# Kernel tuning notes

Hardware: AMD Instinct MI355X
Metric: run time of the kernel (lower is better)

Reference implementation:

```python
import jax, jax.numpy as jnp
import numpy as np

B, S, D, H = 2, 2048, 1024, 16
HD = D // H          # 64
ROT = HD // 2        # 32

def _rope(x, cos, sin):
    # x: [B,S,H,HD] -> pairs [B,S,H,ROT,2]; cos/sin: [S,ROT] -> [1,S,1,ROT]
    x2 = x.reshape(x.shape[:3] + (ROT, 2))
    x0, x1 = x2[..., 0], x2[..., 1]
    c = cos[None, :, None, :]
    s = sin[None, :, None, :]
    out = jnp.stack([x0 * c - x1 * s, x1 * c + x0 * s], axis=-1)
    return out.reshape(x.shape)

def setup_inputs() -> dict:
    key = jax.random.key(0)
    ks = jax.random.split(key, 5)
    hidden_states = jax.random.normal(ks[0], (B, S, D), dtype=jnp.float32)
    # proper rotary cos/sin table: [S, ROT, 2]
    inv_freq = 1.0 / (10000.0 ** (np.arange(0, ROT, dtype=np.float32) / ROT))
    t = np.arange(S, dtype=np.float32)
    ang = np.outer(t, inv_freq)  # [S, ROT]
    freqs = jnp.asarray(np.stack([np.cos(ang), np.sin(ang)], axis=-1), dtype=jnp.float32)
    sc = 1.0 / np.sqrt(D)
    wq = jax.random.normal(ks[1], (D, D), dtype=jnp.float32) * sc
    wk = jax.random.normal(ks[2], (D, D), dtype=jnp.float32) * sc
    wv = jax.random.normal(ks[3], (D, D), dtype=jnp.float32) * sc
    wo = jax.random.normal(ks[4], (D, D), dtype=jnp.float32) * sc
    return {"hidden_states": hidden_states, "freqs": freqs, "wq": wq, "wk": wk, "wv": wv, "wo": wo}

def reference(hidden_states, freqs, wq, wk, wv, wo):
    b, s, _ = hidden_states.shape
    scaling = HD ** -0.5
    q = (hidden_states @ wq.T).reshape(b, s, H, HD)
    k = (hidden_states @ wk.T).reshape(b, s, H, HD)
    v = (hidden_states @ wv.T).reshape(b, s, H, HD)
    cos, sin = freqs[:s, :, 0], freqs[:s, :, 1]
    q = _rope(q, cos, sin)
    k = _rope(k, cos, sin)
    # [B,H,S,S] scores, fp32 softmax
    scores = jnp.einsum('bqhd,bkhd->bhqk', q, k) * scaling
    attn = jax.nn.softmax(scores.astype(jnp.float32), axis=-1).astype(q.dtype)
    out = jnp.einsum('bhqk,bkhd->bqhd', attn, v).reshape(b, s, D)
    return out @ wo.T
```

## Files before the change

kernel.cpp:

```cpp
#include <hip/hip_runtime.h>
#include <hip/hip_bf16.h>

typedef __attribute__((ext_vector_type(8))) short bf16x8;
typedef __attribute__((ext_vector_type(4))) float f32x4;
typedef __attribute__((ext_vector_type(16))) float f32x16;
typedef __attribute__((ext_vector_type(2))) float f32x2;
typedef unsigned short u16;

#define Bc   2
#define Sc   2048
#define Dc   1024
#define Hc   16
#define HDc  64
#define ROTc 32
#define Mrows 4096

__device__ __forceinline__ u16 f2bf(float x) {
  union { float f; unsigned u; } v{x};
  unsigned r = v.u + 0x7fffu + ((v.u >> 16) & 1u);
  return (u16)(r >> 16);
}
__device__ __forceinline__ float bf2f(u16 x) {
  union { unsigned u; float f; } v{(unsigned)x << 16};
  return v.f;
}
__device__ __forceinline__ unsigned cvtpk(float a, float b) {
  unsigned r;
  asm("v_cvt_pk_bf16_f32 %0, %1, %2" : "=v"(r) : "v"(a), "v"(b));
  return r;
}
__device__ __forceinline__ f32x2 pmax2(f32x2 a, f32x2 b) {
  f32x2 r;
  r.x = fmaxf(a.x, b.x);
  r.y = fmaxf(a.y, b.y);
  return r;
}

__device__ __forceinline__ void gload_lds16(const void* g, void* l) {
  __builtin_amdgcn_global_load_lds(
      (const __attribute__((address_space(1))) void*)g,
      (__attribute__((address_space(3))) void*)l, 16, 0, 0);
}

__global__ void cvt_all(const float* __restrict__ h, const float* __restrict__ q,
                        const float* __restrict__ k, const float* __restrict__ v,
                        const float* __restrict__ o,
                        u16* __restrict__ hb, u16* __restrict__ qb, u16* __restrict__ kb,
                        u16* __restrict__ vb, u16* __restrict__ ob) {
  size_t i = ((size_t)blockIdx.x * 256 + threadIdx.x) * 4;
  const float* s;
  u16* d;
  size_t off;
  if (i < (size_t)Mrows * Dc) {
    s = h; d = hb; off = i;
  } else {
    size_t j = i - (size_t)Mrows * Dc;
    int w = (int)(j >> 20);
    off = j & ((1u << 20) - 1);
    s = (w == 0) ? q : (w == 1) ? k : (w == 2) ? v : o;
    d = (w == 0) ? qb : (w == 1) ? kb : (w == 2) ? vb : ob;
  }
  float4 val = *reinterpret_cast<const float4*>(s + off);
  u16 r0 = f2bf(val.x), r1 = f2bf(val.y), r2 = f2bf(val.z), r3 = f2bf(val.w);
  ushort4 outv = {r0, r1, r2, r3};
  *reinterpret_cast<ushort4*>(d + off) = outv;
}

__global__ void gemm_qkv(const u16* __restrict__ A, const u16* __restrict__ W0,
                         const u16* __restrict__ W1, const u16* __restrict__ W2,
                         const float* __restrict__ freqs,
                         u16* __restrict__ Qo, u16* __restrict__ Ko,
                         u16* __restrict__ Vo) {
  __shared__ u16 As[128 * 32];
  __shared__ u16 Bs[128 * 32];
  const int by = blockIdx.y;
  const int wsel = by >> 3;
  const int n0 = (by & 7) * 128;
  const int m0 = blockIdx.x * 128;
  const u16* Bm = (wsel == 0) ? W0 : (wsel == 1) ? W1 : W2;
  const int t = threadIdx.x;
  const int w = t >> 6;
  const int lane = t & 63;
  const int wm = w >> 1, wn = w & 1;
  const int c = lane & 15, g = lane >> 4;
  const int srow = t >> 2, skoff = (t & 3) * 8;

  f32x4 acc[4][4] = {};

  const u16* ag = A + (size_t)(m0 + srow) * Dc + skoff;
  const u16* bg = Bm + (size_t)(n0 + srow) * Dc + skoff;
  u16* al = &As[(w * 16) * 32];
  u16* bl = &Bs[(w * 16) * 32];

  for (int k0 = 0; k0 < Dc; k0 += 32) {
    gload_lds16(ag + k0, al);
    gload_lds16(ag + k0 + (size_t)64 * Dc, al + 64 * 32);
    gload_lds16(bg + k0, bl);
    gload_lds16(bg + k0 + (size_t)64 * Dc, bl + 64 * 32);
    __syncthreads();
    bf16x8 a[4], b[4];
#pragma unroll
    for (int f = 0; f < 4; ++f) {
      a[f] = *(const bf16x8*)&As[(wm * 64 + f * 16 + c) * 32 + g * 8];
      b[f] = *(const bf16x8*)&Bs[(wn * 64 + f * 16 + c) * 32 + g * 8];
    }
#pragma unroll
    for (int fm = 0; fm < 4; ++fm)
#pragma unroll
      for (int fn = 0; fn < 4; ++fn)
        acc[fm][fn] =
            __builtin_amdgcn_mfma_f32_16x16x32_bf16(a[fm], b[fn], acc[fm][fn], 0, 0, 0);
    __syncthreads();
  }

  u16* dst = (wsel == 0) ? Qo : (wsel == 1) ? Ko : Vo;
  const float qsc = (wsel == 0) ? 0.125f * 1.44269504f : 1.0f;
  const int codd = c & 1;
#pragma unroll
  for (int fm = 0; fm < 4; ++fm)
#pragma unroll
    for (int fn = 0; fn < 4; ++fn)
#pragma unroll
      for (int r = 0; r < 4; ++r) {
        const int m = m0 + wm * 64 + fm * 16 + g * 4 + r;
        const int n = n0 + wn * 64 + fn * 16 + c;
        float v = acc[fm][fn][r];
        const int b = m >> 11, s = m & (Sc - 1);
        const int hh = n >> 6, d = n & 63;
        size_t idx;
        if (wsel < 2) {
          const float other = __shfl_xor(v, 1);
          const float2 f = reinterpret_cast<const float2*>(freqs)[s * ROTc + (d >> 1)];
          v = codd ? (v * f.x + other * f.y) : (v * f.x - other * f.y);
          v *= qsc;
          idx = (((size_t)(b * Hc + hh) * Sc) + s) * HDc + d;
        } else {
          idx = ((size_t)(b * Hc + hh) * HDc + d) * Sc + s;
        }
        dst[idx] = f2bf(v);
      }
}

__global__ void gemm_out(const u16* __restrict__ A, const u16* __restrict__ Bm,
                         float* __restrict__ C) {
  __shared__ u16 As[64 * 32];
  __shared__ u16 Bs[128 * 32];
  const int m0 = blockIdx.x * 64;
  const int n0 = blockIdx.y * 128;
  const int t = threadIdx.x;
  const int w = t >> 6;
  const int lane = t & 63;
  const int wm = w >> 1, wn = w & 1;
  const int c = lane & 15, g = lane >> 4;
  const int srow = t >> 2, skoff = (t & 3) * 8;

  f32x4 acc[2][4] = {};

  const u16* ag = A + (size_t)(m0 + srow) * Dc + skoff;
  const u16* bg = Bm + (size_t)(n0 + srow) * Dc + skoff;
  u16* al = &As[(w * 16) * 32];
  u16* bl = &Bs[(w * 16) * 32];

  for (int k0 = 0; k0 < Dc; k0 += 32) {
    gload_lds16(ag + k0, al);
    gload_lds16(bg + k0, bl);
    gload_lds16(bg + k0 + (size_t)64 * Dc, bl + 64 * 32);
    __syncthreads();
    bf16x8 a[2], b[4];
#pragma unroll
    for (int f = 0; f < 2; ++f)
      a[f] = *(const bf16x8*)&As[(wm * 32 + f * 16 + c) * 32 + g * 8];
#pragma unroll
    for (int f = 0; f < 4; ++f)
      b[f] = *(const bf16x8*)&Bs[(wn * 64 + f * 16 + c) * 32 + g * 8];
#pragma unroll
    for (int fm = 0; fm < 2; ++fm)
#pragma unroll
      for (int fn = 0; fn < 4; ++fn)
        acc[fm][fn] =
            __builtin_amdgcn_mfma_f32_16x16x32_bf16(a[fm], b[fn], acc[fm][fn], 0, 0, 0);
    __syncthreads();
  }

#pragma unroll
  for (int fm = 0; fm < 2; ++fm)
#pragma unroll
    for (int fn = 0; fn < 4; ++fn)
#pragma unroll
      for (int r = 0; r < 4; ++r) {
        const int m = m0 + wm * 32 + fm * 16 + g * 4 + r;
        const int n = n0 + wn * 64 + fn * 16 + c;
        C[(size_t)m * Dc + n] = acc[fm][fn][r];
      }
}

__global__ __launch_bounds__(512, 2) void flash_attn(
    const u16* __restrict__ Q, const u16* __restrict__ Kb,
    const u16* __restrict__ Vt, u16* __restrict__ Ob) {
  __shared__ u16 smem[32768];
  const int orig = blockIdx.x;
  const int wg = (orig & 7) * 64 + (orig >> 3);
  const int bh = wg >> 4;
  const int q0 = (wg & 15) * 128;
  const int t = threadIdx.x, w = t >> 6, lane = t & 63;
  const int grp = w >> 2, wl = w & 3;
  const int ts = t & 255;
  const int l31 = lane & 31, hi = lane >> 5;
  const int sr = ts >> 4;
  const int su = (ts & 15) ^ (sr & 15);
  const int skv = sr + ((su >> 3) << 5);
  const int sd8 = (su & 7) * 8;
  const int rsw = (l31 & 15);

  const u16* Qp = Q + (size_t)bh * Sc * HDc;
  const u16* Kp = Kb + (size_t)bh * Sc * HDc;
  const u16* Vp = Vt + (size_t)bh * HDc * Sc;
  u16* const Kg = smem + grp * 8192;
  u16* const Vg = smem + 16384 + grp * 8192;

  const int q = q0 + wl * 32 + l31;
  bf16x8 aq[4];
#pragma unroll
  for (int kd = 0; kd < 4; ++kd)
    aq[kd] = *(const bf16x8*)(Qp + (size_t)q * HDc + kd * 16 + hi * 8);

  float m_run = -1e30f, l_run = 0.f;
  f32x16 o0 = {}, o1 = {};

  auto STAGE = [&](int tile, int bb) {
    const int base = grp * 1024 + tile * 64;
    gload_lds16(Kp + (size_t)(base + skv) * HDc + sd8, Kg + bb * 4096 + wl * 512);
    gload_lds16(Kp + (size_t)(base + skv + 16) * HDc + sd8,
                Kg + bb * 4096 + 2048 + wl * 512);
    gload_lds16(Vp + (size_t)skv * Sc + base + sd8, Vg + bb * 4096 + wl * 512);
    gload_lds16(Vp + (size_t)(skv + 16) * Sc + base + sd8,
                Vg + bb * 4096 + 2048 + wl * 512);
  };

  STAGE(0, 0);
  __syncthreads();

  int buf = 0;
  for (int tt = 0; tt < 16; ++tt) {
    if (tt + 1 < 16) STAGE(tt + 1, buf ^ 1);
    const u16* kb2 = Kg + buf * 4096;
    const u16* vb2 = Vg + buf * 4096;
    f32x16 s0 = {}, s1 = {};
    __builtin_amdgcn_s_setprio(1);
#pragma unroll
    for (int kd = 0; kd < 4; ++kd) {
      const int u0 = kd * 2 + hi;
      bf16x8 a0 = *(const bf16x8*)&kb2[l31 * 128 + (u0 ^ rsw) * 8];
      bf16x8 a1 = *(const bf16x8*)&kb2[l31 * 128 + ((u0 + 8) ^ rsw) * 8];
      s0 = __builtin_amdgcn_mfma_f32_32x32x16_bf16(a0, aq[kd], s0, 0, 0, 0);
      s1 = __builtin_amdgcn_mfma_f32_32x32x16_bf16(a1, aq[kd], s1, 0, 0, 0);
    }
    __builtin_amdgcn_s_setprio(0);
    f32x2 t4[4];
#pragma unroll
    for (int i = 0; i < 4; ++i) {
      f32x2 e0; e0.x = s0[2 * i]; e0.y = s0[2 * i + 1];
      f32x2 e1; e1.x = s0[2 * i + 8]; e1.y = s0[2 * i + 9];
      f32x2 e2; e2.x = s1[2 * i]; e2.y = s1[2 * i + 1];
      f32x2 e3; e3.x = s1[2 * i + 8]; e3.y = s1[2 * i + 9];
      t4[i] = pmax2(pmax2(e0, e1), pmax2(e2, e3));
    }
    f32x2 tp = pmax2(pmax2(t4[0], t4[1]), pmax2(t4[2], t4[3]));
    float mt = fmaxf(tp.x, tp.y);
    mt = fmaxf(mt, __shfl_xor(mt, 32));
    const bool skip = __all(mt <= m_run + 8.0f);
    if (!skip) {
      const float mn2 = fmaxf(m_run, mt);
      const float scl = __builtin_amdgcn_exp2f(m_run - mn2);
      m_run = mn2;
      l_run *= scl;
      o0 *= scl;
      o1 *= scl;
    }
    const float mn = m_run;
#pragma unroll
    for (int r = 0; r < 16; ++r) {
      s0[r] = __builtin_amdgcn_exp2f(s0[r] - mn);
      s1[r] = __builtin_amdgcn_exp2f(s1[r] - mn);
    }
    f32x2 ac;
    ac.x = 0.f; ac.y = 0.f;
#pragma unroll
    for (int i = 0; i < 8; ++i) {
      f32x2 e0; e0.x = s0[2 * i]; e0.y = s0[2 * i + 1];
      f32x2 e1; e1.x = s1[2 * i]; e1.y = s1[2 * i + 1];
      ac += e0 + e1;
    }
    float rs = ac.x + ac.y;
    rs += __shfl_xor(rs, 32);
    l_run += rs;
    unsigned pk0[8], pk1[8];
#pragma unroll
    for (int B = 0; B < 4; ++B)
#pragma unroll
      for (int s2 = 0; s2 < 2; ++s2) {
        pk0[B * 2 + s2] = cvtpk(s0[4 * B + 2 * s2], s0[4 * B + 2 * s2 + 1]);
        pk1[B * 2 + s2] = cvtpk(s1[4 * B + 2 * s2], s1[4 * B + 2 * s2 + 1]);
      }
#pragma unroll
    for (int ks = 0; ks < 4; ++ks) {
      const unsigned* pk = (ks >> 1) ? pk1 : pk0;
      const int m2 = (ks & 1) * 4;
      const unsigned A0 = pk[m2 + 0], A1 = pk[m2 + 1];
      const unsigned B0 = pk[m2 + 2], B1 = pk[m2 + 3];
      const unsigned L0 = hi ? B0 : A0, L1 = hi ? B1 : A1;
      const unsigned R0 = hi ? A0 : B0, R1 = hi ? A1 : B1;
      const unsigned X0 = __shfl_xor(R0, 32), X1 = __shfl_xor(R1, 32);
      union { unsigned u[4]; bf16x8 v; } bp;
      bp.u[0] = hi ? X0 : L0;
      bp.u[1] = hi ? X1 : L1;
      bp.u[2] = hi ? L0 : X0;
      bp.u[3] = hi ? L1 : X1;
      const int uv = ks * 2 + hi;
      bf16x8 va0 = *(const bf16x8*)&vb2[l31 * 128 + (uv ^ rsw) * 8];
      bf16x8 va1 = *(const bf16x8*)&vb2[l31 * 128 + ((uv + 8) ^ rsw) * 8];
      __builtin_amdgcn_s_setprio(1);
      o0 = __builtin_amdgcn_mfma_f32_32x32x16_bf16(va0, bp.v, o0, 0, 0, 0);
      o1 = __builtin_amdgcn_mfma_f32_32x32x16_bf16(va1, bp.v, o1, 0, 0, 0);
      __builtin_amdgcn_s_setprio(0);
    }
    __syncthreads();
    buf ^= 1;
  }

  float* fl = reinterpret_cast<float*>(smem);
  const int slot = (wl * 64 + lane) * 35;
  if (grp == 1) {
#pragma unroll
    for (int j = 0; j < 16; ++j) fl[slot + j] = o0[j];
#pragma unroll
    for (int j = 0; j < 16; ++j) fl[slot + 16 + j] = o1[j];
    fl[slot + 32] = m_run;
    fl[slot + 33] = l_run;
  }
  __syncthreads();
  if (grp == 0) {
    const float mB = fl[slot + 32], lB = fl[slot + 33];
    const float mx = fmaxf(m_run, mB);
    const float sA = __builtin_amdgcn_exp2f(m_run - mx);
    const float sB = __builtin_amdgcn_exp2f(mB - mx);
    const float rd = 1.0f / (l_run * sA + lB * sB);
    const float cA = sA * rd, cB = sB * rd;
    const int b = bh >> 4, hh = bh & 15;
    u16* orow = Ob + ((size_t)b * Sc + q) * Dc + hh * HDc;
#pragma unroll
    for (int B2 = 0; B2 < 4; ++B2) {
      const float v0 = o0[4 * B2 + 0] * cA + fl[slot + 4 * B2 + 0] * cB;
      const float v1 = o0[4 * B2 + 1] * cA + fl[slot + 4 * B2 + 1] * cB;
      const float v2 = o0[4 * B2 + 2] * cA + fl[slot + 4 * B2 + 2] * cB;
      const float v3 = o0[4 * B2 + 3] * cA + fl[slot + 4 * B2 + 3] * cB;
      uint2 pv;
      pv.x = cvtpk(v0, v1);
      pv.y = cvtpk(v2, v3);
      *reinterpret_cast<uint2*>(orow + 8 * B2 + 4 * hi) = pv;
    }
#pragma unroll
    for (int B2 = 0; B2 < 4; ++B2) {
      const float v0 = o1[4 * B2 + 0] * cA + fl[slot + 16 + 4 * B2 + 0] * cB;
      const float v1 = o1[4 * B2 + 1] * cA + fl[slot + 16 + 4 * B2 + 1] * cB;
      const float v2 = o1[4 * B2 + 2] * cA + fl[slot + 16 + 4 * B2 + 2] * cB;
      const float v3 = o1[4 * B2 + 3] * cA + fl[slot + 16 + 4 * B2 + 3] * cB;
      uint2 pv;
      pv.x = cvtpk(v0, v1);
      pv.y = cvtpk(v2, v3);
      *reinterpret_cast<uint2*>(orow + 32 + 8 * B2 + 4 * hi) = pv;
    }
  }
}

extern "C" void kernel_launch(void* const* d_in, const int* in_sizes, int n_in,
                              void* d_out, int out_size, void* d_ws, size_t ws_size,
                              hipStream_t stream) {
  (void)in_sizes; (void)n_in; (void)out_size; (void)ws_size;
  const float* hidden = (const float*)d_in[0];
  const float* freqs = (const float*)d_in[1];
  const float* wq = (const float*)d_in[2];
  const float* wk = (const float*)d_in[3];
  const float* wv = (const float*)d_in[4];
  const float* wo = (const float*)d_in[5];
  float* out = (float*)d_out;

  char* ws = (char*)d_ws;
  const size_t MB8 = (size_t)Mrows * Dc * 2;
  const size_t WB = (size_t)Dc * Dc * 2;
  u16* hb = (u16*)ws;  ws += MB8;
  u16* wqb = (u16*)ws; ws += WB;
  u16* wkb = (u16*)ws; ws += WB;
  u16* wvb = (u16*)ws; ws += WB;
  u16* wob = (u16*)ws; ws += WB;
  u16* qb = (u16*)ws;  ws += MB8;
  u16* kb = (u16*)ws;  ws += MB8;
  u16* vtb = (u16*)ws; ws += MB8;
  u16* ab = (u16*)ws;  ws += MB8;

  cvt_all<<<8192, 256, 0, stream>>>(hidden, wq, wk, wv, wo, hb, wqb, wkb, wvb, wob);
  gemm_qkv<<<dim3(32, 24), 256, 0, stream>>>(hb, wqb, wkb, wvb, freqs, qb, kb, vtb);
  flash_attn<<<512, 512, 0, stream>>>(qb, kb, vtb, ab);
  gemm_out<<<dim3(64, 8), 256, 0, stream>>>(ab, wob, out);
}
```

Baseline: 127.9 us.

## XOR-swizzle LDS tiles in GEMMs and remap QKV grid for XCD locality

Both projection GEMMs now store each 16-byte chunk of a row at an XOR-permuted column slot, keyed on the row's low bits, and read it back with the matching permutation. This is meant to cut LDS bank conflicts when the MFMA fragments are read. The QKV GEMM also moves to a 1-D grid whose block index is remapped so that blocks landing on the same XCD share output-column tiles and neighbouring row tiles, aiming for better L2 reuse of A and W. The remap must stay a bijection over the 768 blocks, and the swizzle must match between the write and read sides.

```diff
diff --git a/kernel.cpp b/kernel.cpp
--- a/kernel.cpp
+++ b/kernel.cpp
@@ -73,17 +73,21 @@
                          u16* __restrict__ Vo) {
   __shared__ u16 As[128 * 32];
   __shared__ u16 Bs[128 * 32];
-  const int by = blockIdx.y;
+  const int orig = blockIdx.x;
+  const int idx = orig >> 3;
+  const int bx = (orig & 7) * 4 + (idx & 3);
+  const int by = idx >> 2;
   const int wsel = by >> 3;
   const int n0 = (by & 7) * 128;
-  const int m0 = blockIdx.x * 128;
+  const int m0 = bx * 128;
   const u16* Bm = (wsel == 0) ? W0 : (wsel == 1) ? W1 : W2;
   const int t = threadIdx.x;
   const int w = t >> 6;
   const int lane = t & 63;
   const int wm = w >> 1, wn = w & 1;
   const int c = lane & 15, g = lane >> 4;
-  const int srow = t >> 2, skoff = (t & 3) * 8;
+  const int srow = t >> 2;
+  const int skoff = ((t & 3) ^ (srow & 3)) * 8;
 
   f32x4 acc[4][4] = {};
 
@@ -101,8 +105,8 @@
     bf16x8 a[4], b[4];
 #pragma unroll
     for (int f = 0; f < 4; ++f) {
-      a[f] = *(const bf16x8*)&As[(wm * 64 + f * 16 + c) * 32 + g * 8];
-      b[f] = *(const bf16x8*)&Bs[(wn * 64 + f * 16 + c) * 32 + g * 8];
+      a[f] = *(const bf16x8*)&As[(wm * 64 + f * 16 + c) * 32 + (g ^ (c & 3)) * 8];
+      b[f] = *(const bf16x8*)&Bs[(wn * 64 + f * 16 + c) * 32 + (g ^ (c & 3)) * 8];
     }
 #pragma unroll
     for (int fm = 0; fm < 4; ++fm)
@@ -127,17 +131,17 @@
         float v = acc[fm][fn][r];
         const int b = m >> 11, s = m & (Sc - 1);
         const int hh = n >> 6, d = n & 63;
-        size_t idx;
+        size_t idx2;
         if (wsel < 2) {
           const float other = __shfl_xor(v, 1);
           const float2 f = reinterpret_cast<const float2*>(freqs)[s * ROTc + (d >> 1)];
           v = codd ? (v * f.x + other * f.y) : (v * f.x - other * f.y);
           v *= qsc;
-          idx = (((size_t)(b * Hc + hh) * Sc) + s) * HDc + d;
+          idx2 = (((size_t)(b * Hc + hh) * Sc) + s) * HDc + d;
         } else {
-          idx = ((size_t)(b * Hc + hh) * HDc + d) * Sc + s;
+          idx2 = ((size_t)(b * Hc + hh) * HDc + d) * Sc + s;
         }
-        dst[idx] = f2bf(v);
+        dst[idx2] = f2bf(v);
       }
 }
 
@@ -152,7 +156,8 @@
   const int lane = t & 63;
   const int wm = w >> 1, wn = w & 1;
   const int c = lane & 15, g = lane >> 4;
-  const int srow = t >> 2, skoff = (t & 3) * 8;
+  const int srow = t >> 2;
+  const int skoff = ((t & 3) ^ (srow & 3)) * 8;
 
   f32x4 acc[2][4] = {};
 
@@ -169,10 +174,10 @@
     bf16x8 a[2], b[4];
 #pragma unroll
     for (int f = 0; f < 2; ++f)
-      a[f] = *(const bf16x8*)&As[(wm * 32 + f * 16 + c) * 32 + g * 8];
+      a[f] = *(const bf16x8*)&As[(wm * 32 + f * 16 + c) * 32 + (g ^ (c & 3)) * 8];
 #pragma unroll
     for (int f = 0; f < 4; ++f)
-      b[f] = *(const bf16x8*)&Bs[(wn * 64 + f * 16 + c) * 32 + g * 8];
+      b[f] = *(const bf16x8*)&Bs[(wn * 64 + f * 16 + c) * 32 + (g ^ (c & 3)) * 8];
 #pragma unroll
     for (int fm = 0; fm < 2; ++fm)
 #pragma unroll
@@ -399,7 +404,7 @@
   u16* ab = (u16*)ws;  ws += MB8;
 
   cvt_all<<<8192, 256, 0, stream>>>(hidden, wq, wk, wv, wo, hb, wqb, wkb, wvb, wob);
-  gemm_qkv<<<dim3(32, 24), 256, 0, stream>>>(hb, wqb, wkb, wvb, freqs, qb, kb, vtb);
+  gemm_qkv<<<768, 256, 0, stream>>>(hb, wqb, wkb, wvb, freqs, qb, kb, vtb);
   flash_attn<<<512, 512, 0, stream>>>(qb, kb, vtb, ab);
   gemm_out<<<dim3(64, 8), 256, 0, stream>>>(ab, wob, out);
 }
```

New measurement: 129.6 us. About the same (+1.3%).
